# Kernel tuning notes

Hardware: AMD Instinct MI355X
Metric: run time of the kernel (lower is better)

Reference implementation:

```python
import jax, jax.numpy as jnp
import numpy as np

TOPK = 10

def setup_inputs() -> dict:
    key = jax.random.key(0)
    k1, k2, k3, k4, k5 = jax.random.split(key, 5)
    B, N, M, d = 256, 64, 64, 32
    return {
        "featureVec": jax.random.normal(k1, (B, N, d), dtype=jnp.float32),
        "contextVec": jax.random.normal(k2, (B, M, d), dtype=jnp.float32),
        "Wq": jax.random.normal(k3, (d, d), dtype=jnp.float32) * 0.05,
        "Wk": jax.random.normal(k4, (d, d), dtype=jnp.float32) * 0.05,
        "Wv": jax.random.normal(k5, (d, M), dtype=jnp.float32) * 0.05,
    }


def _lambda_weight(featureVec, contextVec, Wq, Wk, Wv):
    # Lambda-attention producing weight [B, N, M] (M = contextFeatureNum).
    Q = jnp.einsum("bnd,dk->bnk", featureVec, Wq)                 # [B,N,k]
    K = jax.nn.softmax(jnp.einsum("bmd,dk->bmk", contextVec, Wk), axis=1)
    V = jnp.einsum("bmd,dv->bmv", contextVec, Wv)                 # [B,M,v=M]
    lam = jnp.einsum("bmk,bmv->bkv", K, V)                        # content lambda
    return jnp.einsum("bnk,bkv->bnv", Q, lam)                     # [B,N,M]


def reference(featureVec, contextVec, Wq, Wk, Wv):
    B, N, d = featureVec.shape
    # Outer-product value tensor [B, N, M, d]
    value = featureVec[:, :, None, :] * contextVec[:, None, :, :]
    weight = _lambda_weight(featureVec, contextVec, Wq, Wk, Wv)   # [B,N,M]
    topk_vals, idx = jax.lax.top_k(weight, TOPK)                  # [B,N,topk]
    topk_vals = jax.nn.softmax(topk_vals, axis=2)
    # Gather selected context slots along dim 2, then weighted combine.
    out = jnp.take_along_axis(value, idx[..., None], axis=2)      # [B,N,topk,d]
    out = topk_vals[..., None] * out
    return out.reshape(B, N * TOPK, d)
```

## Files before the change

### kernel.cpp

```cpp
#include <hip/hip_runtime.h>
#include <math.h>

constexpr int Bn = 256;
constexpr int Nn = 64;
constexpr int Mn = 64;
constexpr int Dn = 32;
constexpr int TK = 10;
constexpr int NT = 1024;

__device__ __forceinline__ float exp_np(float x) {
    return (float)exp((double)x);
}
__device__ __forceinline__ unsigned int f2u(float f) {
    unsigned int b = __float_as_uint(f);
    return (b & 0x80000000u) ? ~b : (b | 0x80000000u);
}
__device__ __forceinline__ float u2f(unsigned int u) {
    return __uint_as_float((u & 0x80000000u) ? (u ^ 0x80000000u) : ~u);
}

__global__ __launch_bounds__(NT) void sparse_lambda_attn_kernel(
    const float* __restrict__ fv,
    const float* __restrict__ cv,
    const float* __restrict__ Wq,
    const float* __restrict__ Wk,
    const float* __restrict__ Wv,
    float* __restrict__ out)
{
    #pragma clang fp contract(off)

    __shared__ float fT[Dn][65];
    __shared__ float cT[Dn][65];
    __shared__ float c_lds[Mn][36];
    __shared__ float KpT[Dn][68];
    __shared__ float QmT[Dn][68];
    __shared__ float VwS[Mn][68];
    __shared__ float lamS[Dn][68];
    __shared__ float topw[Nn][TK];
    __shared__ int   topi[Nn][TK];

    const int b    = blockIdx.x;
    const int tid  = threadIdx.x;
    const int lane = tid & 63;
    const int wid  = tid >> 6;

    if (tid < 512) {
        const float4 v = reinterpret_cast<const float4*>(fv + (size_t)b * Nn * Dn)[tid];
        const int n = tid >> 3, d4 = (tid & 7) << 2;
        fT[d4 + 0][n] = v.x; fT[d4 + 1][n] = v.y; fT[d4 + 2][n] = v.z; fT[d4 + 3][n] = v.w;
    } else {
        const int t = tid - 512;
        const float4 v = reinterpret_cast<const float4*>(cv + (size_t)b * Mn * Dn)[t];
        const int m = t >> 3, d4 = (t & 7) << 2;
        *reinterpret_cast<float4*>(&c_lds[m][d4]) = v;
        cT[d4 + 0][m] = v.x; cT[d4 + 1][m] = v.y; cT[d4 + 2][m] = v.z; cT[d4 + 3][m] = v.w;
    }
    __syncthreads();

    if (wid < 8) {
        const int kq = __builtin_amdgcn_readfirstlane(wid);
        const int m = lane;
        const float* wkq = Wk + (kq << 2);
        float a0 = 0.f, a1 = 0.f, a2 = 0.f, a3 = 0.f;
        #pragma unroll 4
        for (int d = 0; d < Dn; ++d) {
            const float cc = cT[d][m];
            const float* wr = wkq + d * Dn;
            const float w0 = wr[0], w1 = wr[1], w2 = wr[2], w3 = wr[3];
            a0 = a0 + cc * w0;  a1 = a1 + cc * w1;  a2 = a2 + cc * w2;  a3 = a3 + cc * w3;
        }
        float m0 = a0, m1 = a1, m2 = a2, m3 = a3;
        #pragma unroll
        for (int off = 1; off < 64; off <<= 1) {
            m0 = fmaxf(m0, __shfl_xor(m0, off));
            m1 = fmaxf(m1, __shfl_xor(m1, off));
            m2 = fmaxf(m2, __shfl_xor(m2, off));
            m3 = fmaxf(m3, __shfl_xor(m3, off));
        }
        const float e0 = exp_np(a0 - m0);
        const float e1 = exp_np(a1 - m1);
        const float e2 = exp_np(a2 - m2);
        const float e3 = exp_np(a3 - m3);
        float s0 = 0.f, s1 = 0.f, s2 = 0.f, s3 = 0.f;
        #pragma unroll
        for (int t = 0; t < 64; ++t) {
            s0 = s0 + __shfl(e0, t);
            s1 = s1 + __shfl(e1, t);
            s2 = s2 + __shfl(e2, t);
            s3 = s3 + __shfl(e3, t);
        }
        KpT[(kq << 2) + 0][m] = e0 / s0;
        KpT[(kq << 2) + 1][m] = e1 / s1;
        KpT[(kq << 2) + 2][m] = e2 / s2;
        KpT[(kq << 2) + 3][m] = e3 / s3;
    } else {
        const int q = __builtin_amdgcn_readfirstlane(wid - 8);
        const int nm = lane;
        const float* wqq = Wq + (q << 2);
        const float* wvq = Wv + (q << 3);
        float a0 = 0.f, a1 = 0.f, a2 = 0.f, a3 = 0.f;
        float b0 = 0.f, b1 = 0.f, b2 = 0.f, b3 = 0.f, b4 = 0.f, b5 = 0.f, b6 = 0.f, b7 = 0.f;
        #pragma unroll 4
        for (int d = 0; d < Dn; ++d) {
            const float ff = fT[d][nm];
            const float cc = cT[d][nm];
            const float* wr = wqq + d * Dn;
            const float* ur = wvq + d * Mn;
            const float w0 = wr[0], w1 = wr[1], w2 = wr[2], w3 = wr[3];
            const float u0 = ur[0], u1 = ur[1], u2 = ur[2], u3 = ur[3];
            const float u4 = ur[4], u5 = ur[5], u6 = ur[6], u7 = ur[7];
            a0 = a0 + ff * w0;  a1 = a1 + ff * w1;  a2 = a2 + ff * w2;  a3 = a3 + ff * w3;
            b0 = b0 + cc * u0;  b1 = b1 + cc * u1;  b2 = b2 + cc * u2;  b3 = b3 + cc * u3;
            b4 = b4 + cc * u4;  b5 = b5 + cc * u5;  b6 = b6 + cc * u6;  b7 = b7 + cc * u7;
        }
        QmT[(q << 2) + 0][nm] = a0;
        QmT[(q << 2) + 1][nm] = a1;
        QmT[(q << 2) + 2][nm] = a2;
        QmT[(q << 2) + 3][nm] = a3;
        float4 r0; r0.x = b0; r0.y = b1; r0.z = b2; r0.w = b3;
        float4 r1; r1.x = b4; r1.y = b5; r1.z = b6; r1.w = b7;
        *reinterpret_cast<float4*>(&VwS[nm][(q << 3) + 0]) = r0;
        *reinterpret_cast<float4*>(&VwS[nm][(q << 3) + 4]) = r1;
    }
    __syncthreads();

    if (tid < 512) {
        const int k = tid >> 4, v4 = (tid & 15) << 2;
        float a0 = 0.f, a1 = 0.f, a2 = 0.f, a3 = 0.f;
        for (int m = 0; m < Mn; ++m) {
            const float kk = KpT[k][m];
            const float4 vv = *reinterpret_cast<const float4*>(&VwS[m][v4]);
            a0 = a0 + kk * vv.x;  a1 = a1 + kk * vv.y;  a2 = a2 + kk * vv.z;  a3 = a3 + kk * vv.w;
        }
        float4 r; r.x = a0; r.y = a1; r.z = a2; r.w = a3;
        *reinterpret_cast<float4*>(&lamS[k][v4]) = r;
    }
    __syncthreads();

    {
        const int n = tid >> 4, v4 = (tid & 15) << 2;
        float a0 = 0.f, a1 = 0.f, a2 = 0.f, a3 = 0.f;
        for (int k = 0; k < Dn; ++k) {
            const float qq = QmT[k][n];
            const float4 lv = *reinterpret_cast<const float4*>(&lamS[k][v4]);
            a0 = a0 + qq * lv.x;  a1 = a1 + qq * lv.y;  a2 = a2 + qq * lv.z;  a3 = a3 + qq * lv.w;
        }
        float4 r; r.x = a0; r.y = a1; r.z = a2; r.w = a3;
        *reinterpret_cast<float4*>(&VwS[n][v4]) = r;
    }
    __syncthreads();

    {
        const int g = tid & 15;
        const int n = tid >> 4;

        const float4 s4 = *reinterpret_cast<const float4*>(&VwS[n][g << 2]);
        unsigned su0 = f2u(s4.x), su1 = f2u(s4.y), su2 = f2u(s4.z), su3 = f2u(s4.w);
        unsigned avail = 0xFu;

        float val0 = 0.f, myval = 0.f;
        int   myidx = 0;

        #pragma unroll
        for (int t = 0; t < TK; ++t) {
            unsigned bu = 0u; int bm = 64;
            if ((avail & 1u) && su0 > bu) { bu = su0; bm = (g << 2) + 0; }
            if ((avail & 2u) && su1 > bu) { bu = su1; bm = (g << 2) + 1; }
            if ((avail & 4u) && su2 > bu) { bu = su2; bm = (g << 2) + 2; }
            if ((avail & 8u) && su3 > bu) { bu = su3; bm = (g << 2) + 3; }
            #pragma unroll
            for (int off = 1; off <= 8; off <<= 1) {
                const unsigned ou = __shfl_xor(bu, off);
                const int      om = __shfl_xor(bm, off);
                if (ou > bu || (ou == bu && om < bm)) { bu = ou; bm = om; }
            }
            const float bv = u2f(bu);
            if (t == 0) val0 = bv;
            if (g == t) { myval = bv; myidx = bm; }
            if ((bm >> 2) == g) avail &= ~(1u << (bm & 3));
        }

        const float ev_own = (g < TK) ? exp_np(myval - val0) : 0.f;
        float s = 0.f;
        #pragma unroll
        for (int t = 0; t < TK; ++t) {
            const float e = __shfl(ev_own, (lane & 48) + t);
            s = s + e;
        }
        if (g < TK) {
            topw[n][g] = ev_own / s;
            topi[n][g] = myidx;
        }
    }
    __syncthreads();

    float* ob = out + (size_t)b * (Nn * TK * Dn);
    constexpr int TOT4 = Nn * TK * Dn / 4;
    for (int i = tid; i < TOT4; i += NT) {
        const int n = i / (TK * Dn / 4);
        const int r = i - n * (TK * Dn / 4);
        const int t = r >> 3;
        const int d4 = (r & 7) << 2;
        const float w = topw[n][t];
        const int m = topi[n][t];
        const float f0 = fT[d4 + 0][n];
        const float f1 = fT[d4 + 1][n];
        const float f2 = fT[d4 + 2][n];
        const float f3 = fT[d4 + 3][n];
        const float4 c4 = *reinterpret_cast<const float4*>(&c_lds[m][d4]);
        float4 o;
        { const float vx = f0 * c4.x; o.x = w * vx; }
        { const float vy = f1 * c4.y; o.y = w * vy; }
        { const float vz = f2 * c4.z; o.z = w * vz; }
        { const float vw = f3 * c4.w; o.w = w * vw; }
        reinterpret_cast<float4*>(ob)[i] = o;
    }
}

extern "C" void kernel_launch(void* const* d_in, const int* in_sizes, int n_in,
                              void* d_out, int out_size, void* d_ws, size_t ws_size,
                              hipStream_t stream) {
    const float* fv = (const float*)d_in[0];
    const float* cv = (const float*)d_in[1];
    const float* Wq = (const float*)d_in[2];
    const float* Wk = (const float*)d_in[3];
    const float* Wv = (const float*)d_in[4];
    float* out = (float*)d_out;

    sparse_lambda_attn_kernel<<<Bn, NT, 0, stream>>>(fv, cv, Wq, Wk, Wv, out);
}
```

Before: 27.55 us.

## Split fused kernel into lambda kernel and per-row-chunk output kernel

Splits the single per-batch kernel into two launches. The first computes Q and the content lambda per batch and writes them to the workspace. The second launches four blocks per batch, each covering 16 rows, to do the weight matmul, top-k, softmax and gather-write, which spreads the output-writing phase across more CUs. This adds a second launch plus a global-memory round trip for Q and lambda. It falls back to the monolithic kernel when the workspace is too small.

```diff
diff --git a/kernel.cpp b/kernel.cpp
--- a/kernel.cpp
+++ b/kernel.cpp
@@ -6,7 +6,6 @@
 constexpr int Mn = 64;
 constexpr int Dn = 32;
 constexpr int TK = 10;
-constexpr int NT = 1024;
 
 __device__ __forceinline__ float exp_np(float x) {
     return (float)exp((double)x);
@@ -19,30 +18,25 @@
     return __uint_as_float((u & 0x80000000u) ? (u ^ 0x80000000u) : ~u);
 }
 
-__global__ __launch_bounds__(NT) void sparse_lambda_attn_kernel(
-    const float* __restrict__ fv,
-    const float* __restrict__ cv,
-    const float* __restrict__ Wq,
-    const float* __restrict__ Wk,
-    const float* __restrict__ Wv,
-    float* __restrict__ out)
+__global__ __launch_bounds__(1024) void lam_kernel(
+    const float* __restrict__ fv, const float* __restrict__ cv,
+    const float* __restrict__ Wq, const float* __restrict__ Wk,
+    const float* __restrict__ Wv, float* __restrict__ ws)
 {
     #pragma clang fp contract(off)
 
     __shared__ float fT[Dn][65];
     __shared__ float cT[Dn][65];
-    __shared__ float c_lds[Mn][36];
     __shared__ float KpT[Dn][68];
-    __shared__ float QmT[Dn][68];
     __shared__ float VwS[Mn][68];
-    __shared__ float lamS[Dn][68];
-    __shared__ float topw[Nn][TK];
-    __shared__ int   topi[Nn][TK];
 
     const int b    = blockIdx.x;
     const int tid  = threadIdx.x;
     const int lane = tid & 63;
     const int wid  = tid >> 6;
+
+    float* wsQ = ws + (size_t)b * 4096;
+    float* wsL = wsQ + 2048;
 
     if (tid < 512) {
         const float4 v = reinterpret_cast<const float4*>(fv + (size_t)b * Nn * Dn)[tid];
@@ -52,7 +46,6 @@
         const int t = tid - 512;
         const float4 v = reinterpret_cast<const float4*>(cv + (size_t)b * Mn * Dn)[t];
         const int m = t >> 3, d4 = (t & 7) << 2;
-        *reinterpret_cast<float4*>(&c_lds[m][d4]) = v;
         cT[d4 + 0][m] = v.x; cT[d4 + 1][m] = v.y; cT[d4 + 2][m] = v.z; cT[d4 + 3][m] = v.w;
     }
     __syncthreads();
@@ -113,10 +106,10 @@
             b0 = b0 + cc * u0;  b1 = b1 + cc * u1;  b2 = b2 + cc * u2;  b3 = b3 + cc * u3;
             b4 = b4 + cc * u4;  b5 = b5 + cc * u5;  b6 = b6 + cc * u6;  b7 = b7 + cc * u7;
         }
-        QmT[(q << 2) + 0][nm] = a0;
-        QmT[(q << 2) + 1][nm] = a1;
-        QmT[(q << 2) + 2][nm] = a2;
-        QmT[(q << 2) + 3][nm] = a3;
+        wsQ[((q << 2) + 0) * 64 + nm] = a0;
+        wsQ[((q << 2) + 1) * 64 + nm] = a1;
+        wsQ[((q << 2) + 2) * 64 + nm] = a2;
+        wsQ[((q << 2) + 3) * 64 + nm] = a3;
         float4 r0; r0.x = b0; r0.y = b1; r0.z = b2; r0.w = b3;
         float4 r1; r1.x = b4; r1.y = b5; r1.z = b6; r1.w = b7;
         *reinterpret_cast<float4*>(&VwS[nm][(q << 3) + 0]) = r0;
@@ -124,40 +117,86 @@
     }
     __syncthreads();
 
-    if (tid < 512) {
-        const int k = tid >> 4, v4 = (tid & 15) << 2;
-        float a0 = 0.f, a1 = 0.f, a2 = 0.f, a3 = 0.f;
+    {
+        const int k = tid >> 5;
+        const int v2 = (tid & 31) << 1;
+        float a0 = 0.f, a1 = 0.f;
         for (int m = 0; m < Mn; ++m) {
             const float kk = KpT[k][m];
-            const float4 vv = *reinterpret_cast<const float4*>(&VwS[m][v4]);
-            a0 = a0 + kk * vv.x;  a1 = a1 + kk * vv.y;  a2 = a2 + kk * vv.z;  a3 = a3 + kk * vv.w;
-        }
-        float4 r; r.x = a0; r.y = a1; r.z = a2; r.w = a3;
-        *reinterpret_cast<float4*>(&lamS[k][v4]) = r;
-    }
-    __syncthreads();
-
-    {
-        const int n = tid >> 4, v4 = (tid & 15) << 2;
+            const float2 vv = *reinterpret_cast<const float2*>(&VwS[m][v2]);
+            a0 = a0 + kk * vv.x;  a1 = a1 + kk * vv.y;
+        }
+        float2 r; r.x = a0; r.y = a1;
+        *reinterpret_cast<float2*>(&wsL[k * 64 + v2]) = r;
+    }
+}
+
+__global__ __launch_bounds__(256) void out_kernel(
+    const float* __restrict__ fv, const float* __restrict__ cv,
+    const float* __restrict__ ws, float* __restrict__ out)
+{
+    #pragma clang fp contract(off)
+
+    __shared__ float lamB[Dn][64];
+    __shared__ float QsT[Dn][17];
+    __shared__ float c_r[Mn][36];
+    __shared__ float f_r[16][36];
+    __shared__ float topw[16][TK];
+    __shared__ int   topi[16][TK];
+
+    const int bid = blockIdx.x;
+    const int b   = bid >> 2;
+    const int n0  = (bid & 3) << 4;
+    const int tid = threadIdx.x;
+    const int lane = tid & 63;
+
+    const float* wsQ = ws + (size_t)b * 4096;
+    const float* wsL = wsQ + 2048;
+
+    {
+        const float4* L4 = reinterpret_cast<const float4*>(wsL);
+        float4* D4 = reinterpret_cast<float4*>(&lamB[0][0]);
+        D4[tid]       = L4[tid];
+        D4[tid + 256] = L4[tid + 256];
+    }
+    {
+        const float4* C4 = reinterpret_cast<const float4*>(cv + (size_t)b * Mn * Dn);
+        #pragma unroll
+        for (int p = 0; p < 2; ++p) {
+            const int i = tid + (p << 8);
+            const float4 v = C4[i];
+            const int m = i >> 3, d4 = (i & 7) << 2;
+            *reinterpret_cast<float4*>(&c_r[m][d4]) = v;
+        }
+    }
+    {
+        #pragma unroll
+        for (int p = 0; p < 2; ++p) {
+            const int i = tid + (p << 8);
+            const int k = i >> 4, j = i & 15;
+            QsT[k][j] = wsQ[k * 64 + n0 + j];
+        }
+    }
+    if (tid < 128) {
+        const float4 v = reinterpret_cast<const float4*>(fv + (size_t)b * Nn * Dn + (size_t)n0 * Dn)[tid];
+        const int n = tid >> 3, d4 = (tid & 7) << 2;
+        *reinterpret_cast<float4*>(&f_r[n][d4]) = v;
+    }
+    __syncthreads();
+
+    {
+        const int nl = tid >> 4;
+        const int g  = tid & 15;
+        const int v4 = g << 2;
         float a0 = 0.f, a1 = 0.f, a2 = 0.f, a3 = 0.f;
         for (int k = 0; k < Dn; ++k) {
-            const float qq = QmT[k][n];
-            const float4 lv = *reinterpret_cast<const float4*>(&lamS[k][v4]);
+            const float qq = QsT[k][nl];
+            const float4 lv = *reinterpret_cast<const float4*>(&lamB[k][v4]);
             a0 = a0 + qq * lv.x;  a1 = a1 + qq * lv.y;  a2 = a2 + qq * lv.z;  a3 = a3 + qq * lv.w;
         }
-        float4 r; r.x = a0; r.y = a1; r.z = a2; r.w = a3;
-        *reinterpret_cast<float4*>(&VwS[n][v4]) = r;
-    }
-    __syncthreads();
-
-    {
-        const int g = tid & 15;
-        const int n = tid >> 4;
-
-        const float4 s4 = *reinterpret_cast<const float4*>(&VwS[n][g << 2]);
-        unsigned su0 = f2u(s4.x), su1 = f2u(s4.y), su2 = f2u(s4.z), su3 = f2u(s4.w);
+
+        unsigned su0 = f2u(a0), su1 = f2u(a1), su2 = f2u(a2), su3 = f2u(a3);
         unsigned avail = 0xFu;
-
         float val0 = 0.f, myval = 0.f;
         int   myidx = 0;
 
@@ -188,15 +227,200 @@
             s = s + e;
         }
         if (g < TK) {
-            topw[n][g] = ev_own / s;
-            topi[n][g] = myidx;
-        }
+            topw[nl][g] = ev_own / s;
+            topi[nl][g] = myidx;
+        }
+    }
+    __syncthreads();
+
+    float* ob = out + (size_t)b * (Nn * TK * Dn) + (size_t)n0 * (TK * Dn);
+    #pragma unroll
+    for (int p = 0; p < 5; ++p) {
+        const int i = tid + (p << 8);
+        const int n = i / 80;
+        const int r = i - n * 80;
+        const int t = r >> 3;
+        const int d4 = (r & 7) << 2;
+        const float w = topw[n][t];
+        const int m = topi[n][t];
+        const float4 fr = *reinterpret_cast<const float4*>(&f_r[n][d4]);
+        const float4 cr = *reinterpret_cast<const float4*>(&c_r[m][d4]);
+        float4 o;
+        { const float vx = fr.x * cr.x; o.x = w * vx; }
+        { const float vy = fr.y * cr.y; o.y = w * vy; }
+        { const float vz = fr.z * cr.z; o.z = w * vz; }
+        { const float vw = fr.w * cr.w; o.w = w * vw; }
+        reinterpret_cast<float4*>(ob)[i] = o;
+    }
+}
+
+__global__ __launch_bounds__(1024) void sparse_lambda_attn_mono(
+    const float* __restrict__ fv, const float* __restrict__ cv,
+    const float* __restrict__ Wq, const float* __restrict__ Wk,
+    const float* __restrict__ Wv, float* __restrict__ out)
+{
+    #pragma clang fp contract(off)
+    __shared__ float fT[Dn][65];
+    __shared__ float cT[Dn][65];
+    __shared__ float c_lds[Mn][36];
+    __shared__ float KpT[Dn][68];
+    __shared__ float QmT[Dn][68];
+    __shared__ float VwS[Mn][68];
+    __shared__ float lamS[Dn][68];
+    __shared__ float topw[Nn][TK];
+    __shared__ int   topi[Nn][TK];
+
+    const int b    = blockIdx.x;
+    const int tid  = threadIdx.x;
+    const int lane = tid & 63;
+    const int wid  = tid >> 6;
+
+    if (tid < 512) {
+        const float4 v = reinterpret_cast<const float4*>(fv + (size_t)b * Nn * Dn)[tid];
+        const int n = tid >> 3, d4 = (tid & 7) << 2;
+        fT[d4 + 0][n] = v.x; fT[d4 + 1][n] = v.y; fT[d4 + 2][n] = v.z; fT[d4 + 3][n] = v.w;
+    } else {
+        const int t = tid - 512;
+        const float4 v = reinterpret_cast<const float4*>(cv + (size_t)b * Mn * Dn)[t];
+        const int m = t >> 3, d4 = (t & 7) << 2;
+        *reinterpret_cast<float4*>(&c_lds[m][d4]) = v;
+        cT[d4 + 0][m] = v.x; cT[d4 + 1][m] = v.y; cT[d4 + 2][m] = v.z; cT[d4 + 3][m] = v.w;
+    }
+    __syncthreads();
+
+    if (wid < 8) {
+        const int kq = __builtin_amdgcn_readfirstlane(wid);
+        const int m = lane;
+        const float* wkq = Wk + (kq << 2);
+        float a0 = 0.f, a1 = 0.f, a2 = 0.f, a3 = 0.f;
+        #pragma unroll 4
+        for (int d = 0; d < Dn; ++d) {
+            const float cc = cT[d][m];
+            const float* wr = wkq + d * Dn;
+            const float w0 = wr[0], w1 = wr[1], w2 = wr[2], w3 = wr[3];
+            a0 = a0 + cc * w0;  a1 = a1 + cc * w1;  a2 = a2 + cc * w2;  a3 = a3 + cc * w3;
+        }
+        float m0 = a0, m1 = a1, m2 = a2, m3 = a3;
+        #pragma unroll
+        for (int off = 1; off < 64; off <<= 1) {
+            m0 = fmaxf(m0, __shfl_xor(m0, off));
+            m1 = fmaxf(m1, __shfl_xor(m1, off));
+            m2 = fmaxf(m2, __shfl_xor(m2, off));
+            m3 = fmaxf(m3, __shfl_xor(m3, off));
+        }
+        const float e0 = exp_np(a0 - m0);
+        const float e1 = exp_np(a1 - m1);
+        const float e2 = exp_np(a2 - m2);
+        const float e3 = exp_np(a3 - m3);
+        float s0 = 0.f, s1 = 0.f, s2 = 0.f, s3 = 0.f;
+        #pragma unroll
+        for (int t = 0; t < 64; ++t) {
+            s0 = s0 + __shfl(e0, t);
+            s1 = s1 + __shfl(e1, t);
+            s2 = s2 + __shfl(e2, t);
+            s3 = s3 + __shfl(e3, t);
+        }
+        KpT[(kq << 2) + 0][m] = e0 / s0;
+        KpT[(kq << 2) + 1][m] = e1 / s1;
+        KpT[(kq << 2) + 2][m] = e2 / s2;
+        KpT[(kq << 2) + 3][m] = e3 / s3;
+    } else {
+        const int q = __builtin_amdgcn_readfirstlane(wid - 8);
+        const int nm = lane;
+        const float* wqq = Wq + (q << 2);
+        const float* wvq = Wv + (q << 3);
+        float a0 = 0.f, a1 = 0.f, a2 = 0.f, a3 = 0.f;
+        float b0 = 0.f, b1 = 0.f, b2 = 0.f, b3 = 0.f, b4 = 0.f, b5 = 0.f, b6 = 0.f, b7 = 0.f;
+        #pragma unroll 4
+        for (int d = 0; d < Dn; ++d) {
+            const float ff = fT[d][nm];
+            const float cc = cT[d][nm];
+            const float* wr = wqq + d * Dn;
+            const float* ur = wvq + d * Mn;
+            const float w0 = wr[0], w1 = wr[1], w2 = wr[2], w3 = wr[3];
+            const float u0 = ur[0], u1 = ur[1], u2 = ur[2], u3 = ur[3];
+            const float u4 = ur[4], u5 = ur[5], u6 = ur[6], u7 = ur[7];
+            a0 = a0 + ff * w0;  a1 = a1 + ff * w1;  a2 = a2 + ff * w2;  a3 = a3 + ff * w3;
+            b0 = b0 + cc * u0;  b1 = b1 + cc * u1;  b2 = b2 + cc * u2;  b3 = b3 + cc * u3;
+            b4 = b4 + cc * u4;  b5 = b5 + cc * u5;  b6 = b6 + cc * u6;  b7 = b7 + cc * u7;
+        }
+        QmT[(q << 2) + 0][nm] = a0;
+        QmT[(q << 2) + 1][nm] = a1;
+        QmT[(q << 2) + 2][nm] = a2;
+        QmT[(q << 2) + 3][nm] = a3;
+        float4 r0; r0.x = b0; r0.y = b1; r0.z = b2; r0.w = b3;
+        float4 r1; r1.x = b4; r1.y = b5; r1.z = b6; r1.w = b7;
+        *reinterpret_cast<float4*>(&VwS[nm][(q << 3) + 0]) = r0;
+        *reinterpret_cast<float4*>(&VwS[nm][(q << 3) + 4]) = r1;
+    }
+    __syncthreads();
+
+    if (tid < 512) {
+        const int k = tid >> 4, v4 = (tid & 15) << 2;
+        float a0 = 0.f, a1 = 0.f, a2 = 0.f, a3 = 0.f;
+        for (int m = 0; m < Mn; ++m) {
+            const float kk = KpT[k][m];
+            const float4 vv = *reinterpret_cast<const float4*>(&VwS[m][v4]);
+            a0 = a0 + kk * vv.x;  a1 = a1 + kk * vv.y;  a2 = a2 + kk * vv.z;  a3 = a3 + kk * vv.w;
+        }
+        float4 r; r.x = a0; r.y = a1; r.z = a2; r.w = a3;
+        *reinterpret_cast<float4*>(&lamS[k][v4]) = r;
+    }
+    __syncthreads();
+
+    {
+        const int n = tid >> 4, v4 = (tid & 15) << 2;
+        float a0 = 0.f, a1 = 0.f, a2 = 0.f, a3 = 0.f;
+        for (int k = 0; k < Dn; ++k) {
+            const float qq = QmT[k][n];
+            const float4 lv = *reinterpret_cast<const float4*>(&lamS[k][v4]);
+            a0 = a0 + qq * lv.x;  a1 = a1 + qq * lv.y;  a2 = a2 + qq * lv.z;  a3 = a3 + qq * lv.w;
+        }
+        float4 r; r.x = a0; r.y = a1; r.z = a2; r.w = a3;
+        *reinterpret_cast<float4*>(&VwS[n][v4]) = r;
+    }
+    __syncthreads();
+
+    {
+        const int g = tid & 15;
+        const int n = tid >> 4;
+        const float4 s4 = *reinterpret_cast<const float4*>(&VwS[n][g << 2]);
+        unsigned su0 = f2u(s4.x), su1 = f2u(s4.y), su2 = f2u(s4.z), su3 = f2u(s4.w);
+        unsigned avail = 0xFu;
+        float val0 = 0.f, myval = 0.f;
+        int   myidx = 0;
+        #pragma unroll
+        for (int t = 0; t < TK; ++t) {
+            unsigned bu = 0u; int bm = 64;
+            if ((avail & 1u) && su0 > bu) { bu = su0; bm = (g << 2) + 0; }
+            if ((avail & 2u) && su1 > bu) { bu = su1; bm = (g << 2) + 1; }
+            if ((avail & 4u) && su2 > bu) { bu = su2; bm = (g << 2) + 2; }
+            if ((avail & 8u) && su3 > bu) { bu = su3; bm = (g << 2) + 3; }
+            #pragma unroll
+            for (int off = 1; off <= 8; off <<= 1) {
+                const unsigned ou = __shfl_xor(bu, off);
+                const int      om = __shfl_xor(bm, off);
+                if (ou > bu || (ou == bu && om < bm)) { bu = ou; bm = om; }
+            }
+            const float bv = u2f(bu);
+            if (t == 0) val0 = bv;
+            if (g == t) { myval = bv; myidx = bm; }
+            if ((bm >> 2) == g) avail &= ~(1u << (bm & 3));
+        }
+        const float ev_own = (g < TK) ? exp_np(myval - val0) : 0.f;
+        float s = 0.f;
+        #pragma unroll
+        for (int t = 0; t < TK; ++t) {
+            const float e = __shfl(ev_own, (lane & 48) + t);
+            s = s + e;
+        }
+        if (g < TK) { topw[n][g] = ev_own / s; topi[n][g] = myidx; }
     }
     __syncthreads();
 
     float* ob = out + (size_t)b * (Nn * TK * Dn);
     constexpr int TOT4 = Nn * TK * Dn / 4;
-    for (int i = tid; i < TOT4; i += NT) {
+    for (int i = tid; i < TOT4; i += 1024) {
         const int n = i / (TK * Dn / 4);
         const int r = i - n * (TK * Dn / 4);
         const int t = r >> 3;
@@ -227,5 +451,12 @@
     const float* Wv = (const float*)d_in[4];
     float* out = (float*)d_out;
 
-    sparse_lambda_attn_kernel<<<Bn, NT, 0, stream>>>(fv, cv, Wq, Wk, Wv, out);
-}
+    const size_t ws_needed = (size_t)Bn * 4096 * sizeof(float);
+    if (ws_size >= ws_needed) {
+        float* ws = (float*)d_ws;
+        lam_kernel<<<Bn, 1024, 0, stream>>>(fv, cv, Wq, Wk, Wv, ws);
+        out_kernel<<<Bn * 4, 256, 0, stream>>>(fv, cv, ws, out);
+    } else {
+        sparse_lambda_attn_mono<<<Bn, 1024, 0, stream>>>(fv, cv, Wq, Wk, Wv, out);
+    }
+}
```

Result: slower. 36.04 us (+30.8%).

## Split each batch across two 512-thread blocks and stage weights in LDS

Applied to the files above, without the earlier changes.

Launches two blocks per batch, each handling half of the N rows with 512 threads. Each block recomputes the context-side K softmax, V and lambda redundantly. Wq, Wk and Wv are staged in shared memory for vectorized reads instead of scalar global loads. The softmax denominator now comes from a shared-memory column sum rather than 64 shuffles, and the Q·lambda score computation is fused with top-k selection, removing one barrier. The aim is more blocks in flight across the GPU's compute units and cheaper inner loops, at the cost of duplicated per-batch context work.

```diff
diff --git a/kernel.cpp b/kernel.cpp
--- a/kernel.cpp
+++ b/kernel.cpp
@@ -6,7 +6,8 @@
 constexpr int Mn = 64;
 constexpr int Dn = 32;
 constexpr int TK = 10;
-constexpr int NT = 1024;
+constexpr int NT = 512;
+constexpr int NBLK = Bn * 2;
 
 __device__ __forceinline__ float exp_np(float x) {
     return (float)exp((double)x);
@@ -29,107 +30,129 @@
 {
     #pragma clang fp contract(off)
 
-    __shared__ float fT[Dn][65];
     __shared__ float cT[Dn][65];
-    __shared__ float c_lds[Mn][36];
-    __shared__ float KpT[Dn][68];
-    __shared__ float QmT[Dn][68];
-    __shared__ float VwS[Mn][68];
+    __shared__ float fTh[Dn][33];
+    __shared__ float c_row[Mn][36];
+    __shared__ float wqS[Dn][Dn];
+    __shared__ float wkS[Dn][Dn];
+    __shared__ float wvS[Dn][Mn];
+    __shared__ float KpT[Dn][65];
+    __shared__ float QmT[Dn][33];
+    __shared__ float Vs[Mn][68];
     __shared__ float lamS[Dn][68];
-    __shared__ float topw[Nn][TK];
-    __shared__ int   topi[Nn][TK];
-
-    const int b    = blockIdx.x;
+    __shared__ float topw[32][TK];
+    __shared__ int   topi[32][TK];
+
+    const int bid  = blockIdx.x;
+    const int b    = bid >> 1;
+    const int n0   = (bid & 1) << 5;
     const int tid  = threadIdx.x;
     const int lane = tid & 63;
     const int wid  = tid >> 6;
 
-    if (tid < 512) {
-        const float4 v = reinterpret_cast<const float4*>(fv + (size_t)b * Nn * Dn)[tid];
+    {
+        const float4 v = reinterpret_cast<const float4*>(cv + (size_t)b * Mn * Dn)[tid];
+        const int m = tid >> 3, d4 = (tid & 7) << 2;
+        *reinterpret_cast<float4*>(&c_row[m][d4]) = v;
+        cT[d4 + 0][m] = v.x; cT[d4 + 1][m] = v.y; cT[d4 + 2][m] = v.z; cT[d4 + 3][m] = v.w;
+    }
+    if (tid < 256) {
+        const float4 v = reinterpret_cast<const float4*>(fv + (size_t)b * Nn * Dn)[(n0 << 3) + tid];
         const int n = tid >> 3, d4 = (tid & 7) << 2;
-        fT[d4 + 0][n] = v.x; fT[d4 + 1][n] = v.y; fT[d4 + 2][n] = v.z; fT[d4 + 3][n] = v.w;
-    } else {
-        const int t = tid - 512;
-        const float4 v = reinterpret_cast<const float4*>(cv + (size_t)b * Mn * Dn)[t];
-        const int m = t >> 3, d4 = (t & 7) << 2;
-        *reinterpret_cast<float4*>(&c_lds[m][d4]) = v;
-        cT[d4 + 0][m] = v.x; cT[d4 + 1][m] = v.y; cT[d4 + 2][m] = v.z; cT[d4 + 3][m] = v.w;
-    }
-    __syncthreads();
-
-    if (wid < 8) {
-        const int kq = __builtin_amdgcn_readfirstlane(wid);
+        fTh[d4 + 0][n] = v.x; fTh[d4 + 1][n] = v.y; fTh[d4 + 2][n] = v.z; fTh[d4 + 3][n] = v.w;
+    }
+    {
+        if (tid < 256) reinterpret_cast<float4*>(&wqS[0][0])[tid] = reinterpret_cast<const float4*>(Wq)[tid];
+        else           reinterpret_cast<float4*>(&wkS[0][0])[tid - 256] = reinterpret_cast<const float4*>(Wk)[tid - 256];
+        reinterpret_cast<float4*>(&wvS[0][0])[tid] = reinterpret_cast<const float4*>(Wv)[tid];
+    }
+    __syncthreads();
+
+    if (wid < 4) {
+        const int c0 = wid << 3;
         const int m = lane;
-        const float* wkq = Wk + (kq << 2);
-        float a0 = 0.f, a1 = 0.f, a2 = 0.f, a3 = 0.f;
-        #pragma unroll 4
+        float a0=0.f,a1=0.f,a2=0.f,a3=0.f,a4=0.f,a5=0.f,a6=0.f,a7=0.f;
+        #pragma unroll 8
         for (int d = 0; d < Dn; ++d) {
             const float cc = cT[d][m];
-            const float* wr = wkq + d * Dn;
-            const float w0 = wr[0], w1 = wr[1], w2 = wr[2], w3 = wr[3];
-            a0 = a0 + cc * w0;  a1 = a1 + cc * w1;  a2 = a2 + cc * w2;  a3 = a3 + cc * w3;
-        }
-        float m0 = a0, m1 = a1, m2 = a2, m3 = a3;
+            const float4 w0 = *reinterpret_cast<const float4*>(&wkS[d][c0]);
+            const float4 w1 = *reinterpret_cast<const float4*>(&wkS[d][c0 + 4]);
+            a0 = a0 + cc * w0.x;  a1 = a1 + cc * w0.y;  a2 = a2 + cc * w0.z;  a3 = a3 + cc * w0.w;
+            a4 = a4 + cc * w1.x;  a5 = a5 + cc * w1.y;  a6 = a6 + cc * w1.z;  a7 = a7 + cc * w1.w;
+        }
+        float m0=a0,m1=a1,m2=a2,m3=a3,m4=a4,m5=a5,m6=a6,m7=a7;
         #pragma unroll
         for (int off = 1; off < 64; off <<= 1) {
             m0 = fmaxf(m0, __shfl_xor(m0, off));
             m1 = fmaxf(m1, __shfl_xor(m1, off));
             m2 = fmaxf(m2, __shfl_xor(m2, off));
             m3 = fmaxf(m3, __shfl_xor(m3, off));
-        }
-        const float e0 = exp_np(a0 - m0);
-        const float e1 = exp_np(a1 - m1);
-        const float e2 = exp_np(a2 - m2);
-        const float e3 = exp_np(a3 - m3);
-        float s0 = 0.f, s1 = 0.f, s2 = 0.f, s3 = 0.f;
-        #pragma unroll
-        for (int t = 0; t < 64; ++t) {
-            s0 = s0 + __shfl(e0, t);
-            s1 = s1 + __shfl(e1, t);
-            s2 = s2 + __shfl(e2, t);
-            s3 = s3 + __shfl(e3, t);
-        }
-        KpT[(kq << 2) + 0][m] = e0 / s0;
-        KpT[(kq << 2) + 1][m] = e1 / s1;
-        KpT[(kq << 2) + 2][m] = e2 / s2;
-        KpT[(kq << 2) + 3][m] = e3 / s3;
+            m4 = fmaxf(m4, __shfl_xor(m4, off));
+            m5 = fmaxf(m5, __shfl_xor(m5, off));
+            m6 = fmaxf(m6, __shfl_xor(m6, off));
+            m7 = fmaxf(m7, __shfl_xor(m7, off));
+        }
+        const float e0 = exp_np(a0 - m0), e1 = exp_np(a1 - m1);
+        const float e2 = exp_np(a2 - m2), e3 = exp_np(a3 - m3);
+        const float e4 = exp_np(a4 - m4), e5 = exp_np(a5 - m5);
+        const float e6 = exp_np(a6 - m6), e7 = exp_np(a7 - m7);
+        KpT[c0 + 0][m] = e0; KpT[c0 + 1][m] = e1;
+        KpT[c0 + 2][m] = e2; KpT[c0 + 3][m] = e3;
+        KpT[c0 + 4][m] = e4; KpT[c0 + 5][m] = e5;
+        KpT[c0 + 6][m] = e6; KpT[c0 + 7][m] = e7;
+        float s = 0.f;
+        if (lane < 8) {
+            const int col = c0 + lane;
+            for (int mm = 0; mm < Mn; ++mm) s = s + KpT[col][mm];
+        }
+        const float s0 = __shfl(s, 0), s1 = __shfl(s, 1), s2 = __shfl(s, 2), s3 = __shfl(s, 3);
+        const float s4 = __shfl(s, 4), s5 = __shfl(s, 5), s6 = __shfl(s, 6), s7 = __shfl(s, 7);
+        KpT[c0 + 0][m] = e0 / s0; KpT[c0 + 1][m] = e1 / s1;
+        KpT[c0 + 2][m] = e2 / s2; KpT[c0 + 3][m] = e3 / s3;
+        KpT[c0 + 4][m] = e4 / s4; KpT[c0 + 5][m] = e5 / s5;
+        KpT[c0 + 6][m] = e6 / s6; KpT[c0 + 7][m] = e7 / s7;
     } else {
-        const int q = __builtin_amdgcn_readfirstlane(wid - 8);
-        const int nm = lane;
-        const float* wqq = Wq + (q << 2);
-        const float* wvq = Wv + (q << 3);
-        float a0 = 0.f, a1 = 0.f, a2 = 0.f, a3 = 0.f;
-        float b0 = 0.f, b1 = 0.f, b2 = 0.f, b3 = 0.f, b4 = 0.f, b5 = 0.f, b6 = 0.f, b7 = 0.f;
+        const int q  = wid - 4;
+        const int v0 = q << 4;
+        const int m  = lane;
+        const int nl = lane & 31;
+        const int qc = (q << 3) + ((lane >> 5) << 2);
+        float b0=0.f,b1=0.f,b2=0.f,b3=0.f,b4=0.f,b5=0.f,b6=0.f,b7=0.f;
+        float b8=0.f,b9=0.f,bA=0.f,bB=0.f,bC=0.f,bD=0.f,bE=0.f,bF=0.f;
+        float q0=0.f,q1=0.f,q2=0.f,q3=0.f;
         #pragma unroll 4
         for (int d = 0; d < Dn; ++d) {
-            const float ff = fT[d][nm];
-            const float cc = cT[d][nm];
-            const float* wr = wqq + d * Dn;
-            const float* ur = wvq + d * Mn;
-            const float w0 = wr[0], w1 = wr[1], w2 = wr[2], w3 = wr[3];
-            const float u0 = ur[0], u1 = ur[1], u2 = ur[2], u3 = ur[3];
-            const float u4 = ur[4], u5 = ur[5], u6 = ur[6], u7 = ur[7];
-            a0 = a0 + ff * w0;  a1 = a1 + ff * w1;  a2 = a2 + ff * w2;  a3 = a3 + ff * w3;
-            b0 = b0 + cc * u0;  b1 = b1 + cc * u1;  b2 = b2 + cc * u2;  b3 = b3 + cc * u3;
-            b4 = b4 + cc * u4;  b5 = b5 + cc * u5;  b6 = b6 + cc * u6;  b7 = b7 + cc * u7;
-        }
-        QmT[(q << 2) + 0][nm] = a0;
-        QmT[(q << 2) + 1][nm] = a1;
-        QmT[(q << 2) + 2][nm] = a2;
-        QmT[(q << 2) + 3][nm] = a3;
-        float4 r0; r0.x = b0; r0.y = b1; r0.z = b2; r0.w = b3;
-        float4 r1; r1.x = b4; r1.y = b5; r1.z = b6; r1.w = b7;
-        *reinterpret_cast<float4*>(&VwS[nm][(q << 3) + 0]) = r0;
-        *reinterpret_cast<float4*>(&VwS[nm][(q << 3) + 4]) = r1;
-    }
-    __syncthreads();
-
-    if (tid < 512) {
+            const float cc = cT[d][m];
+            const float ff = fTh[d][nl];
+            const float4 u0 = *reinterpret_cast<const float4*>(&wvS[d][v0]);
+            const float4 u1 = *reinterpret_cast<const float4*>(&wvS[d][v0 + 4]);
+            const float4 u2 = *reinterpret_cast<const float4*>(&wvS[d][v0 + 8]);
+            const float4 u3 = *reinterpret_cast<const float4*>(&wvS[d][v0 + 12]);
+            const float4 wq4 = *reinterpret_cast<const float4*>(&wqS[d][qc]);
+            b0 = b0 + cc * u0.x;  b1 = b1 + cc * u0.y;  b2 = b2 + cc * u0.z;  b3 = b3 + cc * u0.w;
+            b4 = b4 + cc * u1.x;  b5 = b5 + cc * u1.y;  b6 = b6 + cc * u1.z;  b7 = b7 + cc * u1.w;
+            b8 = b8 + cc * u2.x;  b9 = b9 + cc * u2.y;  bA = bA + cc * u2.z;  bB = bB + cc * u2.w;
+            bC = bC + cc * u3.x;  bD = bD + cc * u3.y;  bE = bE + cc * u3.z;  bF = bF + cc * u3.w;
+            q0 = q0 + ff * wq4.x; q1 = q1 + ff * wq4.y; q2 = q2 + ff * wq4.z; q3 = q3 + ff * wq4.w;
+        }
+        float4 r;
+        r.x=b0; r.y=b1; r.z=b2; r.w=b3; *reinterpret_cast<float4*>(&Vs[m][v0 +  0]) = r;
+        r.x=b4; r.y=b5; r.z=b6; r.w=b7; *reinterpret_cast<float4*>(&Vs[m][v0 +  4]) = r;
+        r.x=b8; r.y=b9; r.z=bA; r.w=bB; *reinterpret_cast<float4*>(&Vs[m][v0 +  8]) = r;
+        r.x=bC; r.y=bD; r.z=bE; r.w=bF; *reinterpret_cast<float4*>(&Vs[m][v0 + 12]) = r;
+        QmT[qc + 0][nl] = q0;
+        QmT[qc + 1][nl] = q1;
+        QmT[qc + 2][nl] = q2;
+        QmT[qc + 3][nl] = q3;
+    }
+    __syncthreads();
+
+    {
         const int k = tid >> 4, v4 = (tid & 15) << 2;
         float a0 = 0.f, a1 = 0.f, a2 = 0.f, a3 = 0.f;
         for (int m = 0; m < Mn; ++m) {
             const float kk = KpT[k][m];
-            const float4 vv = *reinterpret_cast<const float4*>(&VwS[m][v4]);
+            const float4 vv = *reinterpret_cast<const float4*>(&Vs[m][v4]);
             a0 = a0 + kk * vv.x;  a1 = a1 + kk * vv.y;  a2 = a2 + kk * vv.z;  a3 = a3 + kk * vv.w;
         }
         float4 r; r.x = a0; r.y = a1; r.z = a2; r.w = a3;
@@ -138,26 +161,18 @@
     __syncthreads();
 
     {
-        const int n = tid >> 4, v4 = (tid & 15) << 2;
+        const int nl = tid >> 4;
+        const int g  = tid & 15;
+        const int v4 = g << 2;
         float a0 = 0.f, a1 = 0.f, a2 = 0.f, a3 = 0.f;
         for (int k = 0; k < Dn; ++k) {
-            const float qq = QmT[k][n];
+            const float qq = QmT[k][nl];
             const float4 lv = *reinterpret_cast<const float4*>(&lamS[k][v4]);
             a0 = a0 + qq * lv.x;  a1 = a1 + qq * lv.y;  a2 = a2 + qq * lv.z;  a3 = a3 + qq * lv.w;
         }
-        float4 r; r.x = a0; r.y = a1; r.z = a2; r.w = a3;
-        *reinterpret_cast<float4*>(&VwS[n][v4]) = r;
-    }
-    __syncthreads();
-
-    {
-        const int g = tid & 15;
-        const int n = tid >> 4;
-
-        const float4 s4 = *reinterpret_cast<const float4*>(&VwS[n][g << 2]);
-        unsigned su0 = f2u(s4.x), su1 = f2u(s4.y), su2 = f2u(s4.z), su3 = f2u(s4.w);
+
+        unsigned su0 = f2u(a0), su1 = f2u(a1), su2 = f2u(a2), su3 = f2u(a3);
         unsigned avail = 0xFu;
-
         float val0 = 0.f, myval = 0.f;
         int   myidx = 0;
 
@@ -188,31 +203,32 @@
             s = s + e;
         }
         if (g < TK) {
-            topw[n][g] = ev_own / s;
-            topi[n][g] = myidx;
-        }
-    }
-    __syncthreads();
-
-    float* ob = out + (size_t)b * (Nn * TK * Dn);
-    constexpr int TOT4 = Nn * TK * Dn / 4;
-    for (int i = tid; i < TOT4; i += NT) {
-        const int n = i / (TK * Dn / 4);
-        const int r = i - n * (TK * Dn / 4);
+            topw[nl][g] = ev_own / s;
+            topi[nl][g] = myidx;
+        }
+    }
+    __syncthreads();
+
+    float* ob = out + (size_t)b * (Nn * TK * Dn) + (size_t)n0 * (TK * Dn);
+    #pragma unroll
+    for (int p = 0; p < 5; ++p) {
+        const int i = tid + (p << 9);
+        const int n = i / 80;
+        const int r = i - n * 80;
         const int t = r >> 3;
         const int d4 = (r & 7) << 2;
         const float w = topw[n][t];
         const int m = topi[n][t];
-        const float f0 = fT[d4 + 0][n];
-        const float f1 = fT[d4 + 1][n];
-        const float f2 = fT[d4 + 2][n];
-        const float f3 = fT[d4 + 3][n];
-        const float4 c4 = *reinterpret_cast<const float4*>(&c_lds[m][d4]);
+        const float f0 = fTh[d4 + 0][n];
+        const float f1 = fTh[d4 + 1][n];
+        const float f2 = fTh[d4 + 2][n];
+        const float f3 = fTh[d4 + 3][n];
+        const float4 cr = *reinterpret_cast<const float4*>(&c_row[m][d4]);
         float4 o;
-        { const float vx = f0 * c4.x; o.x = w * vx; }
-        { const float vy = f1 * c4.y; o.y = w * vy; }
-        { const float vz = f2 * c4.z; o.z = w * vz; }
-        { const float vw = f3 * c4.w; o.w = w * vw; }
+        { const float vx = f0 * cr.x; o.x = w * vx; }
+        { const float vy = f1 * cr.y; o.y = w * vy; }
+        { const float vz = f2 * cr.z; o.z = w * vz; }
+        { const float vw = f3 * cr.w; o.w = w * vw; }
         reinterpret_cast<float4*>(ob)[i] = o;
     }
 }
@@ -227,5 +243,5 @@
     const float* Wv = (const float*)d_in[4];
     float* out = (float*)d_out;
 
-    sparse_lambda_attn_kernel<<<Bn, NT, 0, stream>>>(fv, cv, Wq, Wk, Wv, out);
-}
+    sparse_lambda_attn_kernel<<<NBLK, NT, 0, stream>>>(fv, cv, Wq, Wk, Wv, out);
+}
```

After: 29.57 us. +7.3%, slower.
